# Kernel optimization log

Hardware: AMD Instinct MI355X
Metric: run time of the kernel (lower is better)

## Reference

```python
import jax, jax.numpy as jnp
import numpy as np
from jax import lax

B, S, I, H, O = 2048, 125, 2, 300, 2
NOISE_STD = 0.01


def setup_inputs() -> dict:
    key = jax.random.key(0)
    ks = jax.random.split(key, 8)
    k = 1.0 / np.sqrt(H)  # torch RNNCell / Linear uniform init bound
    return {
        "x": jax.random.normal(ks[0], (B, S, I), dtype=jnp.float32),
        "noise": jax.random.normal(ks[1], (B, S, H), dtype=jnp.float32),
        "W_ih": jax.random.uniform(ks[2], (H, I), jnp.float32, -k, k),
        "b_ih": jax.random.uniform(ks[3], (H,), jnp.float32, -k, k),
        "W_hh": jax.random.uniform(ks[4], (H, H), jnp.float32, -k, k),
        "b_hh": jax.random.uniform(ks[5], (H,), jnp.float32, -k, k),
        "W_out": jax.random.uniform(ks[6], (O, H), jnp.float32, -k, k),
        "b_out": jax.random.uniform(ks[7], (O,), jnp.float32, -k, k),
    }


def reference(x, noise, W_ih, b_ih, W_hh, b_hh, W_out, b_out):
    # x: [B,S,I], noise: [B,S,H]
    batch = x.shape[0]
    hidden = W_hh.shape[0]
    # Precompute the input-to-hidden projection for all timesteps at once.
    xin = jnp.einsum("bsi,hi->sbh", x, W_ih) + b_ih  # [S,B,H]
    noise_t = jnp.swapaxes(noise, 0, 1) * jnp.asarray(NOISE_STD, x.dtype)  # [S,B,H]

    def step(h, inp):
        xt, nt = inp
        # torch RNNCell(relu): h' = relu(x@W_ih^T + b_ih + h@W_hh^T + b_hh)
        h = jax.nn.relu(xt + h @ W_hh.T + b_hh) + nt
        return h, h

    h0 = jnp.zeros((batch, hidden), x.dtype)
    _, hs = lax.scan(step, h0, (xin, noise_t))  # hs: [S,B,H]
    # Per-step output linear, batched over all timesteps.
    out = jnp.einsum("sbh,oh->bso", hs, W_out) + b_out  # [B,S,O]
    return out
```

## Files before the change

kernel.cpp:

```cpp
#include <hip/hip_runtime.h>
#include <stdint.h>


#define SEQ   125
#define HID   300
#define APAD  328
#define KT    10
#define WAVES 10
#define NTH   (WAVES * 64)
#define RPW   8
#define NCH   600
#define NSLAB 2408

typedef __attribute__((ext_vector_type(8))) short bf16x8;
typedef __attribute__((ext_vector_type(4))) float f32x4;

__device__ __forceinline__ short f2bf(float f) {
  union { float f; uint32_t u; } v; v.f = f;
  uint32_t r = (v.u + 0x7fffu + ((v.u >> 16) & 1u)) >> 16;
  return (short)r;
}

__device__ __forceinline__ uint32_t cvt_pk_bf16(float lo, float hi) {
  uint32_t r;
  asm("v_cvt_pk_bf16_f32 %0, %1, %2" : "=v"(r) : "v"(lo), "v"(hi));
  return r;
}

__device__ __forceinline__ void dma16(const float* g, float* l) {
  __builtin_amdgcn_global_load_lds(
      (const __attribute__((address_space(1))) unsigned int*)g,
      (__attribute__((address_space(3))) unsigned int*)l, 16, 0, 0);
}

#define STEP_BARRIER() \
  asm volatile("s_waitcnt vmcnt(1) lgkmcnt(0)\n\ts_barrier" ::: "memory")

__global__ __launch_bounds__(NTH)
__attribute__((amdgpu_waves_per_eu(3, 3)))
void rnn_fused(
    const float* __restrict__ x,
    const float* __restrict__ noise,
    const float* __restrict__ W_ih,
    const float* __restrict__ b_ih,
    const float* __restrict__ W_hh,
    const float* __restrict__ b_hh,
    const float* __restrict__ W_out,
    const float* __restrict__ b_out,
    float* __restrict__ out)
{
  __shared__ __align__(16) short Abuf[2][9][APAD];
  __shared__ __align__(16) float Nbuf[3][NSLAB];
  __shared__ float xbuf[RPW][SEQ * 2];
  __shared__ float outbuf[RPW][SEQ * 2];

  const int tid  = threadIdx.x;
  const int wave = tid >> 6;
  const int lane = tid & 63;
  const int grp  = lane >> 4;
  const int lc   = lane & 15;
  const int row0 = blockIdx.x * RPW;
  const int grp8 = grp * 8;
  const int arow = (lc < 8) ? lc : 8;
  const bool lcr = (lc < 8);
  const bool w9  = (wave == 9);
  const int cb0  = wave * 32 + grp * 4;
  const int nb0  = lc * HID + cb0;

  for (int i = tid; i < 2 * 9 * APAD / 2; i += NTH)
    ((uint32_t*)Abuf)[i] = 0u;
  for (int i = tid; i < RPW * SEQ * 2; i += NTH) {
    int r = i / (SEQ * 2), j = i % (SEQ * 2);
    xbuf[r][j] = x[(row0 + r) * (SEQ * 2) + j];
  }

  const float bout0 = b_out[0], bout1 = b_out[1];

  bf16x8 wf0[KT], wf1[KT];
#pragma unroll
  for (int t = 0; t < 2; ++t) {
    int c = wave * 32 + t * 16 + lc;
#pragma unroll
    for (int kt = 0; kt < KT; ++kt) {
      bf16x8 f;
#pragma unroll
      for (int e = 0; e < 8; ++e) {
        int k = kt * 32 + grp8 + e;
        float v = 0.f;
        if (c < HID) {
          if (k < HID)            v = W_hh[c * HID + k];
          else if (k == HID)      v = W_ih[c * 2 + 0];
          else if (k == HID + 1)  v = W_ih[c * 2 + 1];
          else if (k == HID + 2)  v = b_ih[c] + b_hh[c];
        } else if (c == HID) {
          if (k < HID)            v = W_out[k];
        } else if (c == HID + 1) {
          if (k < HID)            v = W_out[HID + k];
        }
        f[e] = f2bf(v);
      }
      if (t == 0) wf0[kt] = f; else wf1[kt] = f;
    }
  }

  const bool dma = (tid < NCH);
  const float* gsrc = dma
      ? noise + (size_t)(row0 + tid / 75) * (SEQ * HID) + (tid % 75) * 4
      : noise;

  __syncthreads();

  if (tid < 8) {
    float2 xv = *(const float2*)&x[(size_t)(row0 + tid) * (SEQ * 2)];
    *(uint32_t*)&Abuf[0][tid][300] = cvt_pk_bf16(xv.x, xv.y);
    Abuf[0][tid][302] = (short)0x3F80;
    Abuf[1][tid][302] = (short)0x3F80;
  }

  if (dma) {
    dma16(gsrc, &Nbuf[0][wave * 256]);
    dma16(gsrc + HID, &Nbuf[1][wave * 256]);
  }
  const float* gsrc2 = gsrc + 2 * HID;
  STEP_BARRIER();

  const bool xw = (wave == 0) && (grp == 0) && lcr;

#define STEPM(S, CUR, RB, WB, DO_OUT, DO_EPI, DO_X, DO_ADV, DO_DMA)            \
  {                                                                            \
    if (DO_DMA) { if (dma) dma16(gsrc2, &Nbuf[WB][wave * 256]); }              \
    if (DO_ADV) gsrc2 += HID;                                                  \
    const short* Ab = &Abuf[CUR][arow][grp8];                                  \
    f32x4 t0a = {0.f,0.f,0.f,0.f}, t0b = {0.f,0.f,0.f,0.f};                    \
    f32x4 t1a = {0.f,0.f,0.f,0.f}, t1b = {0.f,0.f,0.f,0.f};                    \
    _Pragma("unroll")                                                          \
    for (int kt = 0; kt < KT; kt += 2) {                                       \
      bf16x8 ha = *(const bf16x8*)(Ab + kt * 32);                              \
      bf16x8 hb = *(const bf16x8*)(Ab + kt * 32 + 32);                         \
      t0a = __builtin_amdgcn_mfma_f32_16x16x32_bf16(wf0[kt],     ha, t0a, 0,0,0); \
      t1a = __builtin_amdgcn_mfma_f32_16x16x32_bf16(wf1[kt],     ha, t1a, 0,0,0); \
      t0b = __builtin_amdgcn_mfma_f32_16x16x32_bf16(wf0[kt + 1], hb, t0b, 0,0,0); \
      t1b = __builtin_amdgcn_mfma_f32_16x16x32_bf16(wf1[kt + 1], hb, t1b, 0,0,0); \
    }                                                                          \
    f32x4 ac0 = t0a + t0b, ac1 = t1a + t1b;                                    \
    if (w9) {                                                                  \
      if (DO_OUT) { if (grp == 3 && lcr) {                                     \
        float2 o; o.x = ac0[0] + bout0; o.y = ac0[1] + bout1;                  \
        *(float2*)&outbuf[lc][((S) - 1) * 2] = o;                              \
      } }                                                                      \
      if (DO_EPI) { if (lcr && grp < 3) {                                      \
        float4 nz = *(const float4*)&Nbuf[RB][nb0];                            \
        float h0 = fmaxf(ac0[0], 0.f) + 0.01f * nz.x;                          \
        float h1 = fmaxf(ac0[1], 0.f) + 0.01f * nz.y;                          \
        float h2 = fmaxf(ac0[2], 0.f) + 0.01f * nz.z;                          \
        float h3 = fmaxf(ac0[3], 0.f) + 0.01f * nz.w;                          \
        uint2 pk; pk.x = cvt_pk_bf16(h0, h1); pk.y = cvt_pk_bf16(h2, h3);      \
        *(uint2*)&Abuf[(CUR) ^ 1][lc][cb0] = pk;                               \
      } }                                                                      \
    } else {                                                                   \
      if (DO_EPI) { if (lcr) {                                                 \
        float4 nz0 = *(const float4*)&Nbuf[RB][nb0];                           \
        float4 nz1 = *(const float4*)&Nbuf[RB][nb0 + 16];                      \
        float a0 = fmaxf(ac0[0], 0.f) + 0.01f * nz0.x;                         \
        float a1 = fmaxf(ac0[1], 0.f) + 0.01f * nz0.y;                         \
        float a2 = fmaxf(ac0[2], 0.f) + 0.01f * nz0.z;                         \
        float a3 = fmaxf(ac0[3], 0.f) + 0.01f * nz0.w;                         \
        float b0 = fmaxf(ac1[0], 0.f) + 0.01f * nz1.x;                         \
        float b1 = fmaxf(ac1[1], 0.f) + 0.01f * nz1.y;                         \
        float b2 = fmaxf(ac1[2], 0.f) + 0.01f * nz1.z;                         \
        float b3 = fmaxf(ac1[3], 0.f) + 0.01f * nz1.w;                         \
        uint2 p0; p0.x = cvt_pk_bf16(a0, a1); p0.y = cvt_pk_bf16(a2, a3);      \
        uint2 p1; p1.x = cvt_pk_bf16(b0, b1); p1.y = cvt_pk_bf16(b2, b3);      \
        *(uint2*)&Abuf[(CUR) ^ 1][lc][cb0] = p0;                               \
        *(uint2*)&Abuf[(CUR) ^ 1][lc][cb0 + 16] = p1;                          \
      } }                                                                      \
    }                                                                          \
    if (DO_X) { if (xw) {                                                      \
      float2 xv = *(const float2*)&xbuf[lc][((S) + 1) * 2];                    \
      *(uint32_t*)&Abuf[(CUR) ^ 1][lc][300] = cvt_pk_bf16(xv.x, xv.y);         \
    } }                                                                        \
    if (DO_EPI) STEP_BARRIER();                                                \
  }

  STEPM(0, 0, 0, 2, 0, 1, 1, 1, 1);
  STEPM(1, 1, 1, 0, 1, 1, 1, 1, 1);
  STEPM(2, 0, 2, 1, 1, 1, 1, 1, 1);
  STEPM(3, 1, 0, 2, 1, 1, 1, 1, 1);
  STEPM(4, 0, 1, 0, 1, 1, 1, 1, 1);
  STEPM(5, 1, 2, 1, 1, 1, 1, 1, 1);

  for (int s = 6; s < 120; s += 6) {
    STEPM(s + 0, 0, 0, 2, 1, 1, 1, 1, 1);
    STEPM(s + 1, 1, 1, 0, 1, 1, 1, 1, 1);
    STEPM(s + 2, 0, 2, 1, 1, 1, 1, 1, 1);
    STEPM(s + 3, 1, 0, 2, 1, 1, 1, 1, 1);
    STEPM(s + 4, 0, 1, 0, 1, 1, 1, 1, 1);
    STEPM(s + 5, 1, 2, 1, 1, 1, 1, 1, 1);
  }

  STEPM(120, 0, 0, 2, 1, 1, 1, 1, 1);
  STEPM(121, 1, 1, 0, 1, 1, 1, 1, 1);
  STEPM(122, 0, 2, 1, 1, 1, 1, 0, 1);
  STEPM(123, 1, 0, 2, 1, 1, 1, 0, 1);
  STEPM(124, 0, 1, 0, 1, 1, 0, 0, 1);
  STEPM(125, 1, 2, 1, 1, 0, 0, 0, 0);

#undef STEPM

  __syncthreads();

  for (int i = tid; i < RPW * SEQ * 2; i += NTH) {
    int r = i / (SEQ * 2), j = i % (SEQ * 2);
    out[(row0 + r) * (SEQ * 2) + j] = outbuf[r][j];
  }
}

extern "C" void kernel_launch(void* const* d_in, const int* in_sizes, int n_in,
                              void* d_out, int out_size, void* d_ws, size_t ws_size,
                              hipStream_t stream) {
  const float* xp     = (const float*)d_in[0];
  const float* noise  = (const float*)d_in[1];
  const float* W_ih   = (const float*)d_in[2];
  const float* b_ih   = (const float*)d_in[3];
  const float* W_hh   = (const float*)d_in[4];
  const float* b_hh   = (const float*)d_in[5];
  const float* W_out  = (const float*)d_in[6];
  const float* b_out  = (const float*)d_in[7];
  float* outp         = (float*)d_out;

  rnn_fused<<<dim3(2048 / RPW), dim3(NTH), 0, stream>>>(
      xp, noise, W_ih, b_ih, W_hh, b_hh, W_out, b_out, outp);
}
```

Measured before the change: 141.3 us.

## Load noise directly into registers instead of staging through LDS via DMA

```diff
diff --git a/kernel.cpp b/kernel.cpp
--- a/kernel.cpp
+++ b/kernel.cpp
@@ -9,8 +9,6 @@
 #define WAVES 10
 #define NTH   (WAVES * 64)
 #define RPW   8
-#define NCH   600
-#define NSLAB 2408
 
 typedef __attribute__((ext_vector_type(8))) short bf16x8;
 typedef __attribute__((ext_vector_type(4))) float f32x4;
@@ -27,14 +25,8 @@
   return r;
 }
 
-__device__ __forceinline__ void dma16(const float* g, float* l) {
-  __builtin_amdgcn_global_load_lds(
-      (const __attribute__((address_space(1))) unsigned int*)g,
-      (__attribute__((address_space(3))) unsigned int*)l, 16, 0, 0);
-}
-
 #define STEP_BARRIER() \
-  asm volatile("s_waitcnt vmcnt(1) lgkmcnt(0)\n\ts_barrier" ::: "memory")
+  asm volatile("s_waitcnt lgkmcnt(0)\n\ts_barrier" ::: "memory")
 
 __global__ __launch_bounds__(NTH)
 __attribute__((amdgpu_waves_per_eu(3, 3)))
@@ -50,7 +42,6 @@
     float* __restrict__ out)
 {
   __shared__ __align__(16) short Abuf[2][9][APAD];
-  __shared__ __align__(16) float Nbuf[3][NSLAB];
   __shared__ float xbuf[RPW][SEQ * 2];
   __shared__ float outbuf[RPW][SEQ * 2];
 
@@ -65,7 +56,7 @@
   const bool lcr = (lc < 8);
   const bool w9  = (wave == 9);
   const int cb0  = wave * 32 + grp * 4;
-  const int nb0  = lc * HID + cb0;
+  const int nc0  = (w9 && grp == 3) ? 0 : cb0;
 
   for (int i = tid; i < 2 * 9 * APAD / 2; i += NTH)
     ((uint32_t*)Abuf)[i] = 0u;
@@ -103,11 +94,6 @@
     }
   }
 
-  const bool dma = (tid < NCH);
-  const float* gsrc = dma
-      ? noise + (size_t)(row0 + tid / 75) * (SEQ * HID) + (tid % 75) * 4
-      : noise;
-
   __syncthreads();
 
   if (tid < 8) {
@@ -117,19 +103,18 @@
     Abuf[1][tid][302] = (short)0x3F80;
   }
 
-  if (dma) {
-    dma16(gsrc, &Nbuf[0][wave * 256]);
-    dma16(gsrc + HID, &Nbuf[1][wave * 256]);
-  }
-  const float* gsrc2 = gsrc + 2 * HID;
+  int nidx = (row0 + (lcr ? lc : 0)) * (SEQ * HID) + nc0;
+  float4 nz0 = {0.f, 0.f, 0.f, 0.f}, nz1 = {0.f, 0.f, 0.f, 0.f};
+  if (lcr) nz0 = *(const float4*)&noise[nidx];
+  if (lcr && !w9) nz1 = *(const float4*)&noise[nidx + 16];
+  nidx += HID;
+
   STEP_BARRIER();
 
   const bool xw = (wave == 0) && (grp == 0) && lcr;
 
-#define STEPM(S, CUR, RB, WB, DO_OUT, DO_EPI, DO_X, DO_ADV, DO_DMA)            \
+#define STEPM(S, CUR, DO_OUT, DO_EPI, DO_X, DO_NLD)                            \
   {                                                                            \
-    if (DO_DMA) { if (dma) dma16(gsrc2, &Nbuf[WB][wave * 256]); }              \
-    if (DO_ADV) gsrc2 += HID;                                                  \
     const short* Ab = &Abuf[CUR][arow][grp8];                                  \
     f32x4 t0a = {0.f,0.f,0.f,0.f}, t0b = {0.f,0.f,0.f,0.f};                    \
     f32x4 t1a = {0.f,0.f,0.f,0.f}, t1b = {0.f,0.f,0.f,0.f};                    \
@@ -149,18 +134,15 @@
         *(float2*)&outbuf[lc][((S) - 1) * 2] = o;                              \
       } }                                                                      \
       if (DO_EPI) { if (lcr && grp < 3) {                                      \
-        float4 nz = *(const float4*)&Nbuf[RB][nb0];                            \
-        float h0 = fmaxf(ac0[0], 0.f) + 0.01f * nz.x;                          \
-        float h1 = fmaxf(ac0[1], 0.f) + 0.01f * nz.y;                          \
-        float h2 = fmaxf(ac0[2], 0.f) + 0.01f * nz.z;                          \
-        float h3 = fmaxf(ac0[3], 0.f) + 0.01f * nz.w;                          \
+        float h0 = fmaxf(ac0[0], 0.f) + 0.01f * nz0.x;                         \
+        float h1 = fmaxf(ac0[1], 0.f) + 0.01f * nz0.y;                         \
+        float h2 = fmaxf(ac0[2], 0.f) + 0.01f * nz0.z;                         \
+        float h3 = fmaxf(ac0[3], 0.f) + 0.01f * nz0.w;                         \
         uint2 pk; pk.x = cvt_pk_bf16(h0, h1); pk.y = cvt_pk_bf16(h2, h3);      \
         *(uint2*)&Abuf[(CUR) ^ 1][lc][cb0] = pk;                               \
       } }                                                                      \
     } else {                                                                   \
       if (DO_EPI) { if (lcr) {                                                 \
-        float4 nz0 = *(const float4*)&Nbuf[RB][nb0];                           \
-        float4 nz1 = *(const float4*)&Nbuf[RB][nb0 + 16];                      \
         float a0 = fmaxf(ac0[0], 0.f) + 0.01f * nz0.x;                         \
         float a1 = fmaxf(ac0[1], 0.f) + 0.01f * nz0.y;                         \
         float a2 = fmaxf(ac0[2], 0.f) + 0.01f * nz0.z;                         \
@@ -179,31 +161,36 @@
       float2 xv = *(const float2*)&xbuf[lc][((S) + 1) * 2];                    \
       *(uint32_t*)&Abuf[(CUR) ^ 1][lc][300] = cvt_pk_bf16(xv.x, xv.y);         \
     } }                                                                        \
+    if (DO_NLD) {        \
+      if (lcr) nz0 = *(const float4*)&noise[nidx];                             \
+      if (lcr && !w9) nz1 = *(const float4*)&noise[nidx + 16];                 \
+      nidx += HID;                                                             \
+    }                                                                          \
     if (DO_EPI) STEP_BARRIER();                                                \
   }
 
-  STEPM(0, 0, 0, 2, 0, 1, 1, 1, 1);
-  STEPM(1, 1, 1, 0, 1, 1, 1, 1, 1);
-  STEPM(2, 0, 2, 1, 1, 1, 1, 1, 1);
-  STEPM(3, 1, 0, 2, 1, 1, 1, 1, 1);
-  STEPM(4, 0, 1, 0, 1, 1, 1, 1, 1);
-  STEPM(5, 1, 2, 1, 1, 1, 1, 1, 1);
+  STEPM(0, 0, 0, 1, 1, 1);
+  STEPM(1, 1, 1, 1, 1, 1);
+  STEPM(2, 0, 1, 1, 1, 1);
+  STEPM(3, 1, 1, 1, 1, 1);
+  STEPM(4, 0, 1, 1, 1, 1);
+  STEPM(5, 1, 1, 1, 1, 1);
 
   for (int s = 6; s < 120; s += 6) {
-    STEPM(s + 0, 0, 0, 2, 1, 1, 1, 1, 1);
-    STEPM(s + 1, 1, 1, 0, 1, 1, 1, 1, 1);
-    STEPM(s + 2, 0, 2, 1, 1, 1, 1, 1, 1);
-    STEPM(s + 3, 1, 0, 2, 1, 1, 1, 1, 1);
-    STEPM(s + 4, 0, 1, 0, 1, 1, 1, 1, 1);
-    STEPM(s + 5, 1, 2, 1, 1, 1, 1, 1, 1);
-  }
-
-  STEPM(120, 0, 0, 2, 1, 1, 1, 1, 1);
-  STEPM(121, 1, 1, 0, 1, 1, 1, 1, 1);
-  STEPM(122, 0, 2, 1, 1, 1, 1, 0, 1);
-  STEPM(123, 1, 0, 2, 1, 1, 1, 0, 1);
-  STEPM(124, 0, 1, 0, 1, 1, 0, 0, 1);
-  STEPM(125, 1, 2, 1, 1, 0, 0, 0, 0);
+    STEPM(s + 0, 0, 1, 1, 1, 1);
+    STEPM(s + 1, 1, 1, 1, 1, 1);
+    STEPM(s + 2, 0, 1, 1, 1, 1);
+    STEPM(s + 3, 1, 1, 1, 1, 1);
+    STEPM(s + 4, 0, 1, 1, 1, 1);
+    STEPM(s + 5, 1, 1, 1, 1, 1);
+  }
+
+  STEPM(120, 0, 1, 1, 1, 1);
+  STEPM(121, 1, 1, 1, 1, 1);
+  STEPM(122, 0, 1, 1, 1, 1);
+  STEPM(123, 1, 1, 1, 1, 1);
+  STEPM(124, 0, 1, 1, 0, 0);
+  STEPM(125, 1, 1, 0, 0, 0);
 
 #undef STEPM
 
```

Result: slower. 164.2 us (+16.2%).
